# Kernel tuning notes

Hardware: AMD Instinct MI355X
Metric: run time of the kernel (lower is better)

The kernel has to match this reference:

```python
import jax, jax.numpy as jnp
import numpy as np

NUM_MODES = 64
BATCH = 512


def calc_tensor(num_modes: int) -> np.ndarray:
    # Kronecker-delta selection-rule coupling tensor, shape [M, M, M, M]
    v = np.arange(1, num_modes + 1)
    m, i, j, k = np.meshgrid(v, v, v, v, indexing='ij')
    d = lambda a, b: (a == b).astype(np.int64)
    B = i * j * k ** 2 * (
        d(k + i, m + j) - d(k + i, -(m + j))
        + d(k + i, m - j) - d(k + i, -(m - j))
        + d(k - i, m + j) - d(k - i, -(m + j))
        + d(k - i, m - j) - d(k - i, -(m - j))
    )
    A = 0.5 * np.pi ** 4 * (B + np.transpose(B, (0, 3, 1, 2)) + np.transpose(B, (0, 2, 3, 1)))
    return A.astype(np.float32)


def setup_inputs() -> dict:
    key = jax.random.key(0)
    q = jax.random.normal(key, (BATCH, NUM_MODES), dtype=jnp.float32)
    A = jnp.asarray(calc_tensor(NUM_MODES))  # [M, M, M, M], fixed buffer
    return {"q": q, "A": A}


def reference(q, A):
    # original: q_vec = einsum('bm,bn,bk->mnkb', q, q, q).flatten -> [M^3, B];
    # out = -(A_flat @ q_vec).T  ==  -einsum('mijk,bi,bj,bk->bm', A, q, q, q)
    return -jnp.einsum('mijk,bi,bj,bk->bm', A, q, q, q)
```

## Files before the change

kernel.cpp:

```cpp
#include <hip/hip_runtime.h>


__global__ __launch_bounds__(64) void nsf_kernel(const float* __restrict__ q,
                                                 float* __restrict__ out) {
    const int b = blockIdx.x;
    const int t = threadIdx.x;

    __shared__ float w[64];
    __shared__ float Ue[192];
    __shared__ float Up[256];
    __shared__ float Es[256];

    const float qv = q[b * 64 + t];
    const float fi = (float)(t + 1);
    const float uv = fi * qv;

    Ue[128 + t] = 0.f;
    Up[65 + t]  = 0.f;
    Up[129 + t] = 0.f;
    if (t == 0) { Ue[63] = 0.f; Up[0] = 0.f; }

    w[t] = fi * fi * qv;
    Up[t + 1] = uv;
    Ue[64 + t] = uv;
    if (t <= 62) Ue[62 - t] = uv;
    __syncthreads();

    const int s0 = t + 1;
    float acc0 = 0.f, acc1 = 0.f;
    #pragma unroll
    for (int k = 1; k <= 64; ++k) {
        const float wk = w[k - 1];
        acc0 += wk * (Ue[63 + s0 - k] - Up[k + s0]);
        acc1 += wk * Ue[127 + s0 - k];
    }
    Es[127 + s0] = acc0;
    Es[127 - s0] = -acc0;
    Es[191 + s0] = acc1;
    if (s0 <= 63) Es[63 - s0] = -acc1;
    if (t == 0) Es[127] = 0.f;
    __syncthreads();

    const int m = t + 1;
    float acc = 0.f;
    #pragma unroll
    for (int j = 1; j <= 64; ++j) {
        acc += Up[j] * (Es[127 + m + j] + Es[127 + m - j]);
    }
    const float kconst = -146.11363655100363f;
    out[b * 64 + t] = kconst * acc;
}

extern "C" void kernel_launch(void* const* d_in, const int* in_sizes, int n_in,
                              void* d_out, int out_size, void* d_ws, size_t ws_size,
                              hipStream_t stream) {
    const float* q = (const float*)d_in[0];
    float* out = (float*)d_out;
    const int batch = in_sizes[0] / 64;
    nsf_kernel<<<batch, 64, 0, stream>>>(q, out);
}
```

Baseline: 89.10 us.

## Split per-batch reductions across four waves with shared-memory partial sums

Each block now uses 256 threads, with each of four waves computing a quarter of the k and j reduction loops and combining partials through shared memory. This shortens the serial dependent FMA chain per thread and raises occupancy for the small grid. It adds two extra barriers and shared-memory traffic for partial-sum merging.

```diff
diff --git a/kernel.cpp b/kernel.cpp
--- a/kernel.cpp
+++ b/kernel.cpp
@@ -1,54 +1,76 @@
 #include <hip/hip_runtime.h>
 
 
-__global__ __launch_bounds__(64) void nsf_kernel(const float* __restrict__ q,
-                                                 float* __restrict__ out) {
-    const int b = blockIdx.x;
-    const int t = threadIdx.x;
+__global__ __launch_bounds__(256) void nsf_kernel(const float* __restrict__ q,
+                                                  float* __restrict__ out) {
+    const int b  = blockIdx.x;
+    const int tt = threadIdx.x;
+    const int l  = tt & 63;
+    const int wv = tt >> 6;
 
     __shared__ float w[64];
     __shared__ float Ue[192];
-    __shared__ float Up[256];
+    __shared__ float Up[160];
     __shared__ float Es[256];
+    __shared__ float Ep[512];
+    __shared__ float Cp[256];
 
-    const float qv = q[b * 64 + t];
-    const float fi = (float)(t + 1);
-    const float uv = fi * qv;
-
-    Ue[128 + t] = 0.f;
-    Up[65 + t]  = 0.f;
-    Up[129 + t] = 0.f;
-    if (t == 0) { Ue[63] = 0.f; Up[0] = 0.f; }
-
-    w[t] = fi * fi * qv;
-    Up[t + 1] = uv;
-    Ue[64 + t] = uv;
-    if (t <= 62) Ue[62 - t] = uv;
+    if (wv == 0) {
+        Ue[128 + l] = 0.f;
+    } else if (wv == 1) {
+        Up[65 + l] = 0.f;
+    } else if (wv == 2) {
+        if (l < 31) Up[129 + l] = 0.f;
+        if (l == 31) { Ue[63] = 0.f; Up[0] = 0.f; Es[127] = 0.f; }
+    } else {
+        const float qv = q[b * 64 + l];
+        const float fi = (float)(l + 1);
+        const float uv = fi * qv;
+        w[l] = fi * fi * qv;
+        Up[l + 1] = uv;
+        Ue[64 + l] = uv;
+        if (l <= 62) Ue[62 - l] = uv;
+    }
     __syncthreads();
 
-    const int s0 = t + 1;
+    const int s0 = l + 1;
+    const int k0 = wv * 16 + 1;
     float acc0 = 0.f, acc1 = 0.f;
     #pragma unroll
-    for (int k = 1; k <= 64; ++k) {
+    for (int kk = 0; kk < 16; ++kk) {
+        const int k = k0 + kk;
         const float wk = w[k - 1];
         acc0 += wk * (Ue[63 + s0 - k] - Up[k + s0]);
         acc1 += wk * Ue[127 + s0 - k];
     }
-    Es[127 + s0] = acc0;
-    Es[127 - s0] = -acc0;
-    Es[191 + s0] = acc1;
-    if (s0 <= 63) Es[63 - s0] = -acc1;
-    if (t == 0) Es[127] = 0.f;
+    Ep[wv * 128 + l]      = acc0;
+    Ep[wv * 128 + 64 + l] = acc1;
     __syncthreads();
 
-    const int m = t + 1;
+    if (tt < 128) {
+        const int s = tt + 1;
+        const float e = Ep[tt] + Ep[128 + tt] + Ep[256 + tt] + Ep[384 + tt];
+        Es[127 + s] = e;
+        if (s <= 127) Es[127 - s] = -e;
+    }
+    __syncthreads();
+
+    const int m = l + 1;
+    const int j0 = wv * 16 + 1;
     float acc = 0.f;
     #pragma unroll
-    for (int j = 1; j <= 64; ++j) {
+    for (int jj = 0; jj < 16; ++jj) {
+        const int j = j0 + jj;
         acc += Up[j] * (Es[127 + m + j] + Es[127 + m - j]);
     }
-    const float kconst = -146.11363655100363f;
-    out[b * 64 + t] = kconst * acc;
+    Cp[wv * 64 + l] = acc;
+    __syncthreads();
+
+    if (tt < 64) {
+        const float kconst = -146.11363655100363f;
+        out[b * 64 + tt] = kconst *
+            (Cp[tt] + Cp[64 + tt] + Cp[128 + tt] + Cp[192 + tt]);
+    }
 }
 
 extern "C" void kernel_launch(void* const* d_in, const int* in_sizes, int n_in,
@@ -57,5 +79,5 @@
     const float* q = (const float*)d_in[0];
     float* out = (float*)d_out;
     const int batch = in_sizes[0] / 64;
-    nsf_kernel<<<batch, 64, 0, stream>>>(q, out);
+    nsf_kernel<<<batch, 256, 0, stream>>>(q, out);
 }
```

Measured after the change: 88.51 us. About the same (-0.7%).
